# Optimization experiments

Measured on AMD Instinct MI355X. Metric: run time of the kernel, lower is better.

## Reference

```python
import jax, jax.numpy as jnp
import numpy as np

N = 8192
D = 512
N_SLICE = 64
K = 8
H = 30 * K  # 240


def _gen_k_slice(rng):
    xx = rng.normal(0.0, 1.0, (N_SLICE, K, D))
    slices = np.zeros((N_SLICE, K, D), dtype=np.float64)
    for i in range(N_SLICE):
        _, _, vh = np.linalg.svd(xx[i], full_matrices=False)
        slices[i] = vh
    return slices.astype(np.float32)


def setup_inputs() -> dict:
    key = jax.random.key(0)
    k1, k2, k3, k4, k5, k6, k7 = jax.random.split(key, 7)
    rng = np.random.default_rng(0)
    # conv weights: PyTorch Conv1d default init ~ U(-s, s), s = 1/sqrt(fan_in)
    s1 = 1.0 / np.sqrt(K)
    s3 = 1.0 / np.sqrt(H)
    return {
        "X": jax.random.normal(k1, (N, D), dtype=jnp.float32),
        "Y": jax.random.normal(k2, (N, D), dtype=jnp.float32),
        "X_noise": jax.random.normal(k3, (N, N_SLICE * K), dtype=jnp.float32),
        "thetas": jnp.asarray(_gen_k_slice(rng)),                     # [S, K, D]
        "W1": jax.random.uniform(k4, (N_SLICE, H, K), jnp.float32, -s1, s1),
        "b1": jax.random.uniform(k5, (N_SLICE, H), jnp.float32, -s1, s1),
        "W3": jax.random.uniform(k6, (N_SLICE, H), jnp.float32, -s3, s3),
        "b3": jax.random.uniform(k7, (N_SLICE,), jnp.float32, -s3, s3),
        "sigma_noise": 0,
    }


def _mlp(sample, W1, b1, W3, b3):
    # sample: [N, S, K] -> grouped 1x1 conv k->H, relu, grouped conv H->1
    h1 = jax.nn.relu(jnp.einsum('nsk,shk->nsh', sample, W1) + b1[None])
    return jnp.einsum('nsh,sh->ns', h1, W3) + b3[None]  # [N, S]


def reference(X, Y, X_noise, thetas, W1, b1, W3, b3, sigma_noise):
    # batched per-slice projections (fuses the n_slice matmul loop)
    x_sample = jnp.einsum('nd,skd->nsk', X, thetas)  # [N, S, K]
    y_sample = jnp.einsum('nd,skd->nsk', Y, thetas)
    if sigma_noise > 0:
        x_sample = x_sample + sigma_noise * X_noise.reshape(X.shape[0], N_SLICE, K)
    pred_x = _mlp(x_sample, W1, b1, W3, b3)  # [N, S]
    pred_y = _mlp(y_sample, W1, b1, W3, b3)
    n_y = pred_y.shape[0]
    ret = jnp.mean(pred_x, axis=0) - jax.nn.logsumexp(
        pred_y - jnp.log(jnp.float32(n_y)), axis=0)
    return jnp.mean(-ret)
```

## Files before the change

kernel.cpp:

```cpp
#include <hip/hip_runtime.h>
#include <hip/hip_bf16.h>

#define NROWS 8192
#define DDIM  512
#define NS    64
#define KK    8
#define HH    240
#define LDT   40
#define SP2   72

typedef __attribute__((ext_vector_type(8))) short bf16x8;
typedef __attribute__((ext_vector_type(4))) float f32x4;
typedef __attribute__((ext_vector_type(2))) float f32x2;

__device__ inline unsigned cvt2u(float a, float b) {
    __hip_bfloat162 h = __float22bfloat162_rn(make_float2(a, b));
    unsigned u;
    __builtin_memcpy(&u, &h, sizeof(u));
    return u;
}

__global__ __launch_bounds__(256)
void pack_kernel(const float* __restrict__ W1, const float* __restrict__ Th,
                 ushort* __restrict__ W1b, ushort* __restrict__ Thb)
{
    int i = (blockIdx.x * 256 + threadIdx.x) * 4;
    if (i < 122880) {
        float4 v = *(const float4*)(W1 + i);
        *(uint2*)(W1b + i) = make_uint2(cvt2u(v.x, v.y), cvt2u(v.z, v.w));
    } else {
        int j = i - 122880;
        float4 v = *(const float4*)(Th + j);
        *(uint2*)(Thb + j) = make_uint2(cvt2u(v.x, v.y), cvt2u(v.z, v.w));
    }
}

__global__ __launch_bounds__(256, 4)
void proj_mlp_kernel(const float* __restrict__ X,
                     const float* __restrict__ Y,
                     const float* __restrict__ Xn,
                     const ushort* __restrict__ Thb,
                     const ushort* __restrict__ W1b,
                     const float* __restrict__ b1,
                     const float* __restrict__ W3,
                     const float* __restrict__ sig_p,
                     float* __restrict__ sumx,
                     float* __restrict__ maxy,
                     float* __restrict__ sey)
{
    __shared__ __align__(16) ushort smem[64 * LDT * 2];
    ushort* aT = smem;
    ushort* bT = smem + 64 * LDT;
    ushort* sl = smem;

    const int tid  = threadIdx.x;
    const int w    = __builtin_amdgcn_readfirstlane(tid >> 6);
    const int lane = tid & 63;
    const int bx   = blockIdx.x;
    const int by   = blockIdx.y;

    const bool isX = (bx < 128);
    const int  bxl = isX ? bx : (bx - 128);
    const float*  srcA = (isX ? X : Y) + (size_t)bxl * 64 * DDIM;
    const ushort* srcB = Thb + (size_t)by * 64 * DDIM;

    f32x4 acc[2][2];
#pragma unroll
    for (int m = 0; m < 2; ++m)
#pragma unroll
        for (int n = 0; n < 2; ++n) acc[m][n] = (f32x4){0.f, 0.f, 0.f, 0.f};

    const int wr  = (w >> 1) * 32;
    const int wc  = (w & 1) * 32;
    const int r16 = lane & 15;
    const int hi4 = lane >> 4;
    const int offA = (wr + r16) * LDT + hi4 * 8;
    const int offB = (wc + r16) * LDT + hi4 * 8;

    const int arow0 = tid >> 3,  ac4 = tid & 7;
    const int brow  = tid >> 2,  bh  = tid & 3;

    float4 ra[2];
    uint4  rbv;
#pragma unroll
    for (int i = 0; i < 2; ++i)
        ra[i] = *(const float4*)(srcA + (size_t)(arow0 + i * 32) * DDIM + ac4 * 4);
    rbv = *(const uint4*)(srcB + brow * DDIM + bh * 8);

#pragma unroll 1
    for (int kt = 0; kt < DDIM / 32; ++kt) {
        __syncthreads();
#pragma unroll
        for (int i = 0; i < 2; ++i)
            *(uint2*)(aT + (arow0 + i * 32) * LDT + ac4 * 4) =
                make_uint2(cvt2u(ra[i].x, ra[i].y), cvt2u(ra[i].z, ra[i].w));
        *(uint4*)(bT + brow * LDT + bh * 8) = rbv;
        __syncthreads();

        if (kt + 1 < DDIM / 32) {
            const int k0 = (kt + 1) * 32;
#pragma unroll
            for (int i = 0; i < 2; ++i)
                ra[i] = *(const float4*)(srcA + (size_t)(arow0 + i * 32) * DDIM + k0 + ac4 * 4);
            rbv = *(const uint4*)(srcB + brow * DDIM + k0 + bh * 8);
        }

        bf16x8 af[2], bfv[2];
#pragma unroll
        for (int m = 0; m < 2; ++m) af[m] = *(const bf16x8*)(aT + offA + m * 16 * LDT);
#pragma unroll
        for (int n = 0; n < 2; ++n) bfv[n] = *(const bf16x8*)(bT + offB + n * 16 * LDT);
#pragma unroll
        for (int m = 0; m < 2; ++m)
#pragma unroll
            for (int n = 0; n < 2; ++n)
                acc[m][n] = __builtin_amdgcn_mfma_f32_16x16x32_bf16(af[m], bfv[n], acc[m][n], 0, 0, 0);
    }

    const float sig = *sig_p;
    const bool addnoise = (sig > 0.f) && isX;
    const int n0g = bxl * 64;

    __syncthreads();
#pragma unroll
    for (int m = 0; m < 2; ++m)
#pragma unroll
        for (int n = 0; n < 2; ++n) {
            const int col  = wc + n * 16 + r16;
            const int rowb = wr + m * 16 + hi4 * 4;
            float v[4];
#pragma unroll
            for (int j = 0; j < 4; ++j) {
                v[j] = acc[m][n][j];
                if (addnoise)
                    v[j] = fmaf(sig, Xn[(size_t)(n0g + rowb + j) * (NS * KK) + by * 64 + col], v[j]);
            }
            unsigned u01 = cvt2u(v[0], v[1]);
            unsigned u23 = cvt2u(v[2], v[3]);
            sl[(rowb + 0) * SP2 + col] = (ushort)u01;
            sl[(rowb + 1) * SP2 + col] = (ushort)(u01 >> 16);
            sl[(rowb + 2) * SP2 + col] = (ushort)u23;
            sl[(rowb + 3) * SP2 + col] = (ushort)(u23 >> 16);
        }
    __syncthreads();

#pragma unroll 1
    for (int si = 0; si < 2; ++si) {
        const int sloc = w * 2 + si;
        const int s    = by * 8 + sloc;

        bf16x8 bsamp[4];
#pragma unroll
        for (int nt = 0; nt < 4; ++nt) {
            bf16x8 t = {0, 0, 0, 0, 0, 0, 0, 0};
            if (hi4 == 0)
                t = *(const bf16x8*)(sl + (nt * 16 + r16) * SP2 + sloc * 8);
            bsamp[nt] = t;
        }

        const ushort* w1p = W1b + (size_t)s * HH * KK;
        const float*  b1p = b1 + s * HH;
        const float*  w3p = W3 + s * HH;

        f32x2 pn2[4];
#pragma unroll
        for (int nt = 0; nt < 4; ++nt) pn2[nt] = (f32x2){0.f, 0.f};

#pragma unroll 5
        for (int ht = 0; ht < HH / 16; ++ht) {
            bf16x8 aw = {0, 0, 0, 0, 0, 0, 0, 0};
            if (hi4 == 0)
                aw = *(const bf16x8*)(w1p + (ht * 16 + r16) * 8);
            float4 b4 = *(const float4*)(b1p + ht * 16 + hi4 * 4);
            float4 w4 = *(const float4*)(w3p + ht * 16 + hi4 * 4);
            f32x4 z   = (f32x4){b4.x, b4.y, b4.z, b4.w};
            f32x2 w01 = (f32x2){w4.x, w4.y};
            f32x2 w23 = (f32x2){w4.z, w4.w};
            const f32x2 zero2 = (f32x2){0.f, 0.f};
#pragma unroll
            for (int nt = 0; nt < 4; ++nt) {
                f32x4 t = __builtin_amdgcn_mfma_f32_16x16x32_bf16(aw, bsamp[nt], z, 0, 0, 0);
                f32x2 t01 = (f32x2){t[0], t[1]};
                f32x2 t23 = (f32x2){t[2], t[3]};
                t01 = __builtin_elementwise_max(t01, zero2);
                t23 = __builtin_elementwise_max(t23, zero2);
                pn2[nt] = __builtin_elementwise_fma(t01, w01, pn2[nt]);
                pn2[nt] = __builtin_elementwise_fma(t23, w23, pn2[nt]);
            }
        }

        if (isX) {
            float lsum = 0.f;
#pragma unroll
            for (int nt = 0; nt < 4; ++nt) lsum += pn2[nt].x + pn2[nt].y;
#pragma unroll
            for (int off = 1; off < 64; off <<= 1)
                lsum += __shfl_xor(lsum, off);
            if (lane == 0) sumx[s * 128 + bxl] = lsum;
        } else {
            float p[4];
#pragma unroll
            for (int nt = 0; nt < 4; ++nt) {
                f32x2 v = pn2[nt];
                v.x += __shfl_xor(v.x, 16);
                v.y += __shfl_xor(v.y, 16);
                v.x += __shfl_xor(v.x, 32);
                v.y += __shfl_xor(v.y, 32);
                p[nt] = v.x + v.y;
            }
            float M = fmaxf(fmaxf(p[0], p[1]), fmaxf(p[2], p[3]));
            float se = __expf(p[0] - M) + __expf(p[1] - M)
                     + __expf(p[2] - M) + __expf(p[3] - M);
#pragma unroll
            for (int off = 1; off < 16; off <<= 1) {
                float Mo = __shfl_xor(M, off);
                float so = __shfl_xor(se, off);
                float Mm = fmaxf(M, Mo);
                se = se * __expf(M - Mm) + so * __expf(Mo - Mm);
                M = Mm;
            }
            if (lane == 0) {
                maxy[s * 128 + bxl] = M;
                sey[s * 128 + bxl]  = se;
            }
        }
    }
}

__global__ __launch_bounds__(256)
void final_kernel(const float* __restrict__ sumx,
                  const float* __restrict__ maxy,
                  const float* __restrict__ sey,
                  float* __restrict__ out)
{
    __shared__ float term_s[NS];
    const int tid = threadIdx.x;
    const int s = tid >> 2, q = tid & 3;
    const int base = s * 128 + q * 32;

    float sum = 0.f, M = -3.4e38f;
#pragma unroll 8
    for (int i = 0; i < 32; ++i) {
        sum += sumx[base + i];
        M = fmaxf(M, maxy[base + i]);
    }
    float se = 0.f;
#pragma unroll 8
    for (int i = 0; i < 32; ++i)
        se += sey[base + i] * __expf(maxy[base + i] - M);

#pragma unroll
    for (int off = 1; off < 4; off <<= 1) {
        float Mo = __shfl_xor(M, off);
        float so = __shfl_xor(se, off);
        float su = __shfl_xor(sum, off);
        float Mm = fmaxf(M, Mo);
        se = se * __expf(M - Mm) + so * __expf(Mo - Mm);
        M = Mm;
        sum += su;
    }
    if (q == 0)
        term_s[s] = M + logf(se) - logf((float)NROWS) - sum * (1.0f / (float)NROWS);
    __syncthreads();
    if (tid < 64) {
        float v = term_s[tid];
#pragma unroll
        for (int off = 1; off < 64; off <<= 1) v += __shfl_xor(v, off);
        if (tid == 0) out[0] = v * (1.0f / (float)NS);
    }
}

extern "C" void kernel_launch(void* const* d_in, const int* in_sizes, int n_in,
                              void* d_out, int out_size, void* d_ws, size_t ws_size,
                              hipStream_t stream)
{
    const float* X   = (const float*)d_in[0];
    const float* Y   = (const float*)d_in[1];
    const float* Xn  = (const float*)d_in[2];
    const float* Th  = (const float*)d_in[3];
    const float* W1  = (const float*)d_in[4];
    const float* b1  = (const float*)d_in[5];
    const float* W3  = (const float*)d_in[6];
    const float* sig = (const float*)d_in[8];

    ushort* W1b  = (ushort*)d_ws;
    ushort* Thb  = W1b + 122880;
    float*  sumx = (float*)(Thb + 262144);
    float*  maxy = sumx + NS * 128;
    float*  sey  = maxy + NS * 128;

    pack_kernel<<<(122880 + 262144) / 1024, 256, 0, stream>>>(W1, Th, W1b, Thb);

    dim3 g1(256, 8, 1);
    proj_mlp_kernel<<<g1, 256, 0, stream>>>(X, Y, Xn, Thb, W1b, b1, W3,
                                            sig, sumx, maxy, sey);
    final_kernel<<<1, 256, 0, stream>>>(sumx, maxy, sey, (float*)d_out);
}
```

Before: 68.41 us.

## Double-buffer LDS tiles and widen K step to 64 in projection GEMM

The projection GEMM loop now uses a 64-wide K tile instead of 32 and two LDS buffers. The next tile is stored to the alternate buffer and the following global loads are issued while MFMAs run on the current one, so each iteration needs one barrier instead of two. This halves loop trips and synchronisation and overlaps global latency with compute, at the cost of more registers and four times the LDS. That could lower occupancy under the launch bound of 4 blocks per CU.

```diff
diff --git a/kernel.cpp b/kernel.cpp
--- a/kernel.cpp
+++ b/kernel.cpp
@@ -6,8 +6,10 @@
 #define NS    64
 #define KK    8
 #define HH    240
-#define LDT   40
+#define BK    64
+#define LDT2  72
 #define SP2   72
+#define BUFSZ (64 * LDT2)
 
 typedef __attribute__((ext_vector_type(8))) short bf16x8;
 typedef __attribute__((ext_vector_type(4))) float f32x4;
@@ -48,9 +50,7 @@
                      float* __restrict__ maxy,
                      float* __restrict__ sey)
 {
-    __shared__ __align__(16) ushort smem[64 * LDT * 2];
-    ushort* aT = smem;
-    ushort* bT = smem + 64 * LDT;
+    __shared__ __align__(16) ushort smem[4 * BUFSZ];
     ushort* sl = smem;
 
     const int tid  = threadIdx.x;
@@ -74,54 +74,69 @@
     const int wc  = (w & 1) * 32;
     const int r16 = lane & 15;
     const int hi4 = lane >> 4;
-    const int offA = (wr + r16) * LDT + hi4 * 8;
-    const int offB = (wc + r16) * LDT + hi4 * 8;
-
-    const int arow0 = tid >> 3,  ac4 = tid & 7;
-    const int brow  = tid >> 2,  bh  = tid & 3;
-
-    float4 ra[2];
-    uint4  rbv;
-#pragma unroll
-    for (int i = 0; i < 2; ++i)
-        ra[i] = *(const float4*)(srcA + (size_t)(arow0 + i * 32) * DDIM + ac4 * 4);
-    rbv = *(const uint4*)(srcB + brow * DDIM + bh * 8);
-
-#pragma unroll 1
-    for (int kt = 0; kt < DDIM / 32; ++kt) {
+    const int offA = (wr + r16) * LDT2 + hi4 * 8;
+    const int offB = (wc + r16) * LDT2 + hi4 * 8;
+
+    const int ar = tid >> 4, ac = tid & 15;
+    const int br = tid >> 3, bc = tid & 7;
+
+    float4 ra[4];
+    uint4  rbv[2];
+
+#define LOADA(k0) { _Pragma("unroll") \
+    for (int i = 0; i < 4; ++i) \
+        ra[i] = *(const float4*)(srcA + (size_t)(ar + i * 16) * DDIM + (k0) + ac * 4); }
+#define LOADB(k0) { _Pragma("unroll") \
+    for (int i = 0; i < 2; ++i) \
+        rbv[i] = *(const uint4*)(srcB + (size_t)(br + i * 32) * DDIM + (k0) + bc * 8); }
+#define STORE(buf) { ushort* aw_ = smem + (buf) * 2 * BUFSZ; \
+    _Pragma("unroll") \
+    for (int i = 0; i < 4; ++i) \
+        *(uint2*)(aw_ + (ar + i * 16) * LDT2 + ac * 4) = \
+            make_uint2(cvt2u(ra[i].x, ra[i].y), cvt2u(ra[i].z, ra[i].w)); \
+    ushort* bw_ = aw_ + BUFSZ; \
+    _Pragma("unroll") \
+    for (int i = 0; i < 2; ++i) \
+        *(uint4*)(bw_ + (br + i * 32) * LDT2 + bc * 8) = rbv[i]; }
+
+    LOADA(0); LOADB(0);
+    STORE(0);
+    LOADA(64); LOADB(64);
+    __syncthreads();
+
+#pragma unroll 2
+    for (int kt = 0; kt < 8; ++kt) {
+        const int cur = kt & 1;
+        const ushort* aT = smem + cur * 2 * BUFSZ;
+        const ushort* bT = aT + BUFSZ;
+
+        bf16x8 af[2][2], bfv[2][2];
+#pragma unroll
+        for (int ks = 0; ks < 2; ++ks) {
+#pragma unroll
+            for (int m = 0; m < 2; ++m) {
+                af[ks][m]  = *(const bf16x8*)(aT + offA + m * 16 * LDT2 + ks * 32);
+                bfv[ks][m] = *(const bf16x8*)(bT + offB + m * 16 * LDT2 + ks * 32);
+            }
+        }
+#pragma unroll
+        for (int ks = 0; ks < 2; ++ks)
+#pragma unroll
+            for (int m = 0; m < 2; ++m)
+#pragma unroll
+                for (int n = 0; n < 2; ++n)
+                    acc[m][n] = __builtin_amdgcn_mfma_f32_16x16x32_bf16(
+                        af[ks][m], bfv[ks][n], acc[m][n], 0, 0, 0);
+
+        if (kt < 7) STORE(cur ^ 1);
+        if (kt < 6) { LOADA((kt + 2) * BK); LOADB((kt + 2) * BK); }
         __syncthreads();
-#pragma unroll
-        for (int i = 0; i < 2; ++i)
-            *(uint2*)(aT + (arow0 + i * 32) * LDT + ac4 * 4) =
-                make_uint2(cvt2u(ra[i].x, ra[i].y), cvt2u(ra[i].z, ra[i].w));
-        *(uint4*)(bT + brow * LDT + bh * 8) = rbv;
-        __syncthreads();
-
-        if (kt + 1 < DDIM / 32) {
-            const int k0 = (kt + 1) * 32;
-#pragma unroll
-            for (int i = 0; i < 2; ++i)
-                ra[i] = *(const float4*)(srcA + (size_t)(arow0 + i * 32) * DDIM + k0 + ac4 * 4);
-            rbv = *(const uint4*)(srcB + brow * DDIM + k0 + bh * 8);
-        }
-
-        bf16x8 af[2], bfv[2];
-#pragma unroll
-        for (int m = 0; m < 2; ++m) af[m] = *(const bf16x8*)(aT + offA + m * 16 * LDT);
-#pragma unroll
-        for (int n = 0; n < 2; ++n) bfv[n] = *(const bf16x8*)(bT + offB + n * 16 * LDT);
-#pragma unroll
-        for (int m = 0; m < 2; ++m)
-#pragma unroll
-            for (int n = 0; n < 2; ++n)
-                acc[m][n] = __builtin_amdgcn_mfma_f32_16x16x32_bf16(af[m], bfv[n], acc[m][n], 0, 0, 0);
     }
 
     const float sig = *sig_p;
     const bool addnoise = (sig > 0.f) && isX;
     const int n0g = bxl * 64;
 
-    __syncthreads();
 #pragma unroll
     for (int m = 0; m < 2; ++m)
 #pragma unroll
```

Measured after the change: 89.90 us. 31.4% more time.

## Double-buffer projection LDS tiles and switch MFMA inputs from bf16 to fp16

Applied to the files above, without the earlier changes.

The projection GEMM loop now uses two LDS buffers, so each iteration stores the next tile while computing on the current one, with one barrier per step instead of two. All packed operands change from bf16 with round-to-nearest to fp16 with round-toward-zero (cvt_pkrtz), which is a cheaper conversion. The MLP stage moves from the 16x16x32 instruction with half the lanes zeroed to 16x16x16 f16 MFMA, so less work is wasted on padding. The cost is double the LDS use and a narrower fp16 range, though the values here are small.

```diff
diff --git a/kernel.cpp b/kernel.cpp
--- a/kernel.cpp
+++ b/kernel.cpp
@@ -8,13 +8,15 @@
 #define HH    240
 #define LDT   40
 #define SP2   72
-
-typedef __attribute__((ext_vector_type(8))) short bf16x8;
+#define BUF   (64 * LDT)
+
+typedef __attribute__((ext_vector_type(8))) _Float16 f16x8;
+typedef __attribute__((ext_vector_type(4))) _Float16 f16x4;
 typedef __attribute__((ext_vector_type(4))) float f32x4;
 typedef __attribute__((ext_vector_type(2))) float f32x2;
 
-__device__ inline unsigned cvt2u(float a, float b) {
-    __hip_bfloat162 h = __float22bfloat162_rn(make_float2(a, b));
+__device__ inline unsigned pk2u(float a, float b) {
+    auto h = __builtin_amdgcn_cvt_pkrtz(a, b);
     unsigned u;
     __builtin_memcpy(&u, &h, sizeof(u));
     return u;
@@ -22,16 +24,16 @@
 
 __global__ __launch_bounds__(256)
 void pack_kernel(const float* __restrict__ W1, const float* __restrict__ Th,
-                 ushort* __restrict__ W1b, ushort* __restrict__ Thb)
+                 ushort* __restrict__ W1h, ushort* __restrict__ Thh)
 {
     int i = (blockIdx.x * 256 + threadIdx.x) * 4;
     if (i < 122880) {
         float4 v = *(const float4*)(W1 + i);
-        *(uint2*)(W1b + i) = make_uint2(cvt2u(v.x, v.y), cvt2u(v.z, v.w));
+        *(uint2*)(W1h + i) = make_uint2(pk2u(v.x, v.y), pk2u(v.z, v.w));
     } else {
         int j = i - 122880;
         float4 v = *(const float4*)(Th + j);
-        *(uint2*)(Thb + j) = make_uint2(cvt2u(v.x, v.y), cvt2u(v.z, v.w));
+        *(uint2*)(Thh + j) = make_uint2(pk2u(v.x, v.y), pk2u(v.z, v.w));
     }
 }
 
@@ -39,8 +41,8 @@
 void proj_mlp_kernel(const float* __restrict__ X,
                      const float* __restrict__ Y,
                      const float* __restrict__ Xn,
-                     const ushort* __restrict__ Thb,
-                     const ushort* __restrict__ W1b,
+                     const ushort* __restrict__ Thh,
+                     const ushort* __restrict__ W1h,
                      const float* __restrict__ b1,
                      const float* __restrict__ W3,
                      const float* __restrict__ sig_p,
@@ -48,9 +50,7 @@
                      float* __restrict__ maxy,
                      float* __restrict__ sey)
 {
-    __shared__ __align__(16) ushort smem[64 * LDT * 2];
-    ushort* aT = smem;
-    ushort* bT = smem + 64 * LDT;
+    __shared__ __align__(16) ushort smem[4 * BUF];
     ushort* sl = smem;
 
     const int tid  = threadIdx.x;
@@ -62,7 +62,7 @@
     const bool isX = (bx < 128);
     const int  bxl = isX ? bx : (bx - 128);
     const float*  srcA = (isX ? X : Y) + (size_t)bxl * 64 * DDIM;
-    const ushort* srcB = Thb + (size_t)by * 64 * DDIM;
+    const ushort* srcB = Thh + (size_t)by * 64 * DDIM;
 
     f32x4 acc[2][2];
 #pragma unroll
@@ -82,46 +82,52 @@
 
     float4 ra[2];
     uint4  rbv;
-#pragma unroll
-    for (int i = 0; i < 2; ++i)
-        ra[i] = *(const float4*)(srcA + (size_t)(arow0 + i * 32) * DDIM + ac4 * 4);
-    rbv = *(const uint4*)(srcB + brow * DDIM + bh * 8);
-
-#pragma unroll 1
-    for (int kt = 0; kt < DDIM / 32; ++kt) {
+
+#define LOADA(k0) { _Pragma("unroll") \
+    for (int i = 0; i < 2; ++i) \
+        ra[i] = *(const float4*)(srcA + (size_t)(arow0 + i * 32) * DDIM + (k0) + ac4 * 4); }
+#define LOADB(k0) \
+    rbv = *(const uint4*)(srcB + brow * DDIM + (k0) + bh * 8);
+#define STORE(buf) { ushort* aw_ = smem + (buf) * 2 * BUF; \
+    _Pragma("unroll") \
+    for (int i = 0; i < 2; ++i) \
+        *(uint2*)(aw_ + (arow0 + i * 32) * LDT + ac4 * 4) = \
+            make_uint2(pk2u(ra[i].x, ra[i].y), pk2u(ra[i].z, ra[i].w)); \
+    *(uint4*)(aw_ + BUF + brow * LDT + bh * 8) = rbv; }
+
+    LOADA(0); LOADB(0);
+    STORE(0);
+    LOADA(32); LOADB(32);
+    __syncthreads();
+
+#pragma unroll 2
+    for (int kt = 0; kt < 16; ++kt) {
+        const int cur = kt & 1;
+        const ushort* aT = smem + cur * 2 * BUF;
+        const ushort* bT = aT + BUF;
+
+        f16x8 af[2], bfv[2];
+#pragma unroll
+        for (int m = 0; m < 2; ++m) {
+            af[m]  = *(const f16x8*)(aT + offA + m * 16 * LDT);
+            bfv[m] = *(const f16x8*)(bT + offB + m * 16 * LDT);
+        }
+#pragma unroll
+        for (int m = 0; m < 2; ++m)
+#pragma unroll
+            for (int n = 0; n < 2; ++n)
+                acc[m][n] = __builtin_amdgcn_mfma_f32_16x16x32_f16(
+                    af[m], bfv[n], acc[m][n], 0, 0, 0);
+
+        if (kt < 15) STORE(cur ^ 1);
+        if (kt < 14) { LOADA((kt + 2) * 32); LOADB((kt + 2) * 32); }
         __syncthreads();
-#pragma unroll
-        for (int i = 0; i < 2; ++i)
-            *(uint2*)(aT + (arow0 + i * 32) * LDT + ac4 * 4) =
-                make_uint2(cvt2u(ra[i].x, ra[i].y), cvt2u(ra[i].z, ra[i].w));
-        *(uint4*)(bT + brow * LDT + bh * 8) = rbv;
-        __syncthreads();
-
-        if (kt + 1 < DDIM / 32) {
-            const int k0 = (kt + 1) * 32;
-#pragma unroll
-            for (int i = 0; i < 2; ++i)
-                ra[i] = *(const float4*)(srcA + (size_t)(arow0 + i * 32) * DDIM + k0 + ac4 * 4);
-            rbv = *(const uint4*)(srcB + brow * DDIM + k0 + bh * 8);
-        }
-
-        bf16x8 af[2], bfv[2];
-#pragma unroll
-        for (int m = 0; m < 2; ++m) af[m] = *(const bf16x8*)(aT + offA + m * 16 * LDT);
-#pragma unroll
-        for (int n = 0; n < 2; ++n) bfv[n] = *(const bf16x8*)(bT + offB + n * 16 * LDT);
-#pragma unroll
-        for (int m = 0; m < 2; ++m)
-#pragma unroll
-            for (int n = 0; n < 2; ++n)
-                acc[m][n] = __builtin_amdgcn_mfma_f32_16x16x32_bf16(af[m], bfv[n], acc[m][n], 0, 0, 0);
     }
 
     const float sig = *sig_p;
     const bool addnoise = (sig > 0.f) && isX;
     const int n0g = bxl * 64;
 
-    __syncthreads();
 #pragma unroll
     for (int m = 0; m < 2; ++m)
 #pragma unroll
@@ -135,8 +141,8 @@
                 if (addnoise)
                     v[j] = fmaf(sig, Xn[(size_t)(n0g + rowb + j) * (NS * KK) + by * 64 + col], v[j]);
             }
-            unsigned u01 = cvt2u(v[0], v[1]);
-            unsigned u23 = cvt2u(v[2], v[3]);
+            unsigned u01 = pk2u(v[0], v[1]);
+            unsigned u23 = pk2u(v[2], v[3]);
             sl[(rowb + 0) * SP2 + col] = (ushort)u01;
             sl[(rowb + 1) * SP2 + col] = (ushort)(u01 >> 16);
             sl[(rowb + 2) * SP2 + col] = (ushort)u23;
@@ -149,16 +155,16 @@
         const int sloc = w * 2 + si;
         const int s    = by * 8 + sloc;
 
-        bf16x8 bsamp[4];
+        f16x4 bsamp[4];
 #pragma unroll
         for (int nt = 0; nt < 4; ++nt) {
-            bf16x8 t = {0, 0, 0, 0, 0, 0, 0, 0};
-            if (hi4 == 0)
-                t = *(const bf16x8*)(sl + (nt * 16 + r16) * SP2 + sloc * 8);
+            f16x4 t = {0, 0, 0, 0};
+            if (hi4 < 2)
+                t = *(const f16x4*)(sl + (nt * 16 + r16) * SP2 + sloc * 8 + hi4 * 4);
             bsamp[nt] = t;
         }
 
-        const ushort* w1p = W1b + (size_t)s * HH * KK;
+        const ushort* w1p = W1h + (size_t)s * HH * KK;
         const float*  b1p = b1 + s * HH;
         const float*  w3p = W3 + s * HH;
 
@@ -168,9 +174,9 @@
 
 #pragma unroll 5
         for (int ht = 0; ht < HH / 16; ++ht) {
-            bf16x8 aw = {0, 0, 0, 0, 0, 0, 0, 0};
-            if (hi4 == 0)
-                aw = *(const bf16x8*)(w1p + (ht * 16 + r16) * 8);
+            f16x4 aw = {0, 0, 0, 0};
+            if (hi4 < 2)
+                aw = *(const f16x4*)(w1p + (ht * 16 + r16) * 8 + hi4 * 4);
             float4 b4 = *(const float4*)(b1p + ht * 16 + hi4 * 4);
             float4 w4 = *(const float4*)(w3p + ht * 16 + hi4 * 4);
             f32x4 z   = (f32x4){b4.x, b4.y, b4.z, b4.w};
@@ -179,7 +185,7 @@
             const f32x2 zero2 = (f32x2){0.f, 0.f};
 #pragma unroll
             for (int nt = 0; nt < 4; ++nt) {
-                f32x4 t = __builtin_amdgcn_mfma_f32_16x16x32_bf16(aw, bsamp[nt], z, 0, 0, 0);
+                f32x4 t = __builtin_amdgcn_mfma_f32_16x16x16f16(aw, bsamp[nt], z, 0, 0, 0);
                 f32x2 t01 = (f32x2){t[0], t[1]};
                 f32x2 t23 = (f32x2){t[2], t[3]};
                 t01 = __builtin_elementwise_max(t01, zero2);
@@ -283,16 +289,16 @@
     const float* W3  = (const float*)d_in[6];
     const float* sig = (const float*)d_in[8];
 
-    ushort* W1b  = (ushort*)d_ws;
-    ushort* Thb  = W1b + 122880;
-    float*  sumx = (float*)(Thb + 262144);
+    ushort* W1h  = (ushort*)d_ws;
+    ushort* Thh  = W1h + 122880;
+    float*  sumx = (float*)(Thh + 262144);
     float*  maxy = sumx + NS * 128;
     float*  sey  = maxy + NS * 128;
 
-    pack_kernel<<<(122880 + 262144) / 1024, 256, 0, stream>>>(W1, Th, W1b, Thb);
+    pack_kernel<<<(122880 + 262144) / 1024, 256, 0, stream>>>(W1, Th, W1h, Thh);
 
     dim3 g1(256, 8, 1);
-    proj_mlp_kernel<<<g1, 256, 0, stream>>>(X, Y, Xn, Thb, W1b, b1, W3,
+    proj_mlp_kernel<<<g1, 256, 0, stream>>>(X, Y, Xn, Thh, W1h, b1, W3,
                                             sig, sumx, maxy, sey);
     final_kernel<<<1, 256, 0, stream>>>(sumx, maxy, sey, (float*)d_out);
 }
```

After: 68.67 us. Within noise of the previous version (+0.4%).
